# Kernel tuning notes

Measured on AMD Instinct MI355X. Metric: run time of the kernel, lower is better.

The kernel has to match this reference:

```python
import jax, jax.numpy as jnp
import numpy as np

N_NODES = 100000
N_EDGES = 625000
D_IN = 128
D_OUT = 128


def setup_inputs() -> dict:
    key = jax.random.key(0)
    k1, k2, k3, k4, k5 = jax.random.split(key, 5)
    scale = 1.0 / np.sqrt(D_IN)
    x = jax.random.normal(k1, (N_NODES, D_IN), dtype=jnp.float32)
    edge_index = jax.random.randint(k2, (2, N_EDGES), 0, N_NODES, dtype=jnp.int64)
    W_l = jax.random.normal(k3, (D_IN, D_OUT), dtype=jnp.float32) * scale
    b_l = jax.random.normal(k4, (D_OUT,), dtype=jnp.float32) * scale
    W_r = jax.random.normal(k5, (D_IN, D_OUT), dtype=jnp.float32) * scale
    return {"x": x, "edge_index": edge_index, "W_l": W_l, "b_l": b_l, "W_r": W_r}


def reference(x, edge_index, W_l, b_l, W_r):
    # SAGEConv (mean aggr, no self loops):
    #   out = lin_l(mean_{j in N(i)} x_j) + lin_r(x_i)
    src = edge_index[0]  # message source nodes
    dst = edge_index[1]  # aggregation targets
    n = x.shape[0]
    msgs = x[src]  # [E, D_IN] gather
    agg = jax.ops.segment_sum(msgs, dst, num_segments=n)  # [N, D_IN]
    deg = jax.ops.segment_sum(jnp.ones_like(dst, dtype=x.dtype), dst, num_segments=n)
    mean = agg / jnp.maximum(deg, 1.0)[:, None]  # isolated nodes -> 0
    return mean @ W_l + b_l + x @ W_r
```

## Files before the change

### kernel.cpp

```cpp
#include <hip/hip_runtime.h>


constexpr int N_NODES = 100000;
constexpr int N_EDGES = 625000;
constexpr int D = 128;
constexpr int SCAN_CHUNK = 1024;
constexpr int N_SCAN_BLOCKS = (N_NODES + SCAN_CHUNK - 1) / SCAN_CHUNK;
constexpr int CONV_BLOCKS = N_NODES * D / (512 * 4);

typedef __attribute__((ext_vector_type(8))) short short8;
typedef __attribute__((ext_vector_type(4))) short short4v;
typedef __attribute__((ext_vector_type(4))) float f32x4;

__device__ __forceinline__ unsigned short f2bf(float f) {
    union { float f; unsigned int u; } c; c.f = f;
    unsigned int u = c.u + 0x7fffu + ((c.u >> 16) & 1u);
    return (unsigned short)(u >> 16);
}
__device__ __forceinline__ float bflo(unsigned int v) {
    union { unsigned int u; float f; } c; c.u = v << 16; return c.f;
}
__device__ __forceinline__ float bfhi(unsigned int v) {
    union { unsigned int u; float f; } c; c.u = v & 0xffff0000u; return c.f;
}
__device__ __forceinline__ uint2 pack4(float4 a) {
    uint2 r;
    r.x = (unsigned)f2bf(a.x) | ((unsigned)f2bf(a.y) << 16);
    r.y = (unsigned)f2bf(a.z) | ((unsigned)f2bf(a.w) << 16);
    return r;
}

__global__ __launch_bounds__(256) void zero_cnt(int* __restrict__ cnt)
{
    int i = blockIdx.x * 256 + threadIdx.x;
    if (i < N_NODES / 4) ((uint4*)cnt)[i] = make_uint4(0, 0, 0, 0);
}

__global__ __launch_bounds__(256) void prep_hist(
    const float* __restrict__ x, const float* __restrict__ Wl,
    const float* __restrict__ Wr, const int* __restrict__ dst,
    unsigned short* __restrict__ xb, unsigned short* __restrict__ wT,
    int* __restrict__ cnt)
{
    const int tid = threadIdx.x;
    if (blockIdx.x < CONV_BLOCKS) {
        const float4* xp = (const float4*)x;
        int i1 = blockIdx.x * 512 + tid;
        int i2 = i1 + 256;
        float4 a = xp[i1];
        float4 b = xp[i2];
        ((uint2*)xb)[i1] = pack4(a);
        ((uint2*)xb)[i2] = pack4(b);
    } else {
        int t2 = (blockIdx.x - CONV_BLOCKS) * 256 + tid;
        if (t2 < 4096) {
            int n  = t2 >> 5;
            int k0 = (t2 & 31) * 8;
            short8 v;
            #pragma unroll
            for (int j = 0; j < 8; ++j) {
                int k = k0 + j;
                float f = (k < 128) ? Wl[k * 128 + n] : Wr[(k - 128) * 128 + n];
                v[j] = (short)f2bf(f);
            }
            *(short8*)&wT[n * 256 + k0] = v;
        } else if (t2 < 4096 + N_EDGES) {
            int e = t2 - 4096;
            atomicAdd(&cnt[dst[e]], 1);
        }
    }
}

__global__ __launch_bounds__(256) void csr_hist(
    const int* __restrict__ dst, int* __restrict__ cnt)
{
    int e = blockIdx.x * 256 + threadIdx.x;
    if (e < N_EDGES) atomicAdd(&cnt[dst[e]], 1);
}

__global__ __launch_bounds__(256) void scan_blocks(
    const int* __restrict__ cnt, int* __restrict__ ptr, int* __restrict__ bsums)
{
    __shared__ int sh[256];
    const int t = threadIdx.x;
    const int base = blockIdx.x * SCAN_CHUNK + t * 4;
    int v0 = (base + 0 < N_NODES) ? cnt[base + 0] : 0;
    int v1 = (base + 1 < N_NODES) ? cnt[base + 1] : 0;
    int v2 = (base + 2 < N_NODES) ? cnt[base + 2] : 0;
    int v3 = (base + 3 < N_NODES) ? cnt[base + 3] : 0;
    const int tsum = v0 + v1 + v2 + v3;
    sh[t] = tsum;
    __syncthreads();
    #pragma unroll
    for (int off = 1; off < 256; off <<= 1) {
        int val = (t >= off) ? sh[t - off] : 0;
        __syncthreads();
        sh[t] += val;
        __syncthreads();
    }
    const int texcl = sh[t] - tsum;
    if (t == 255) bsums[blockIdx.x] = sh[255];
    int e0 = texcl, e1 = e0 + v0, e2 = e1 + v1, e3 = e2 + v2;
    if (base + 0 < N_NODES) ptr[base + 0] = e0;
    if (base + 1 < N_NODES) ptr[base + 1] = e1;
    if (base + 2 < N_NODES) ptr[base + 2] = e2;
    if (base + 3 < N_NODES) ptr[base + 3] = e3;
}

__global__ __launch_bounds__(256) void add_offsets_fused(
    int* __restrict__ ptr, int* __restrict__ cursor, const int* __restrict__ bsums)
{
    __shared__ int sh[256];
    const int t = threadIdx.x;
    int v = (t < blockIdx.x) ? bsums[t] : 0;
    sh[t] = v;
    __syncthreads();
    #pragma unroll
    for (int off = 128; off > 0; off >>= 1) {
        if (t < off) sh[t] += sh[t + off];
        __syncthreads();
    }
    const int soff = sh[0];
    const int base = blockIdx.x * SCAN_CHUNK + t * 4;
    #pragma unroll
    for (int j = 0; j < 4; ++j) {
        int i = base + j;
        if (i < N_NODES) {
            int p = ptr[i] + soff;
            ptr[i] = p;
            cursor[i] = p;
        }
    }
    if (blockIdx.x == 0 && t == 0) ptr[N_NODES] = N_EDGES;
}

__global__ __launch_bounds__(256) void csr_fill(
    const int* __restrict__ src, const int* __restrict__ dst,
    int* __restrict__ cursor, int* __restrict__ sorted_src)
{
    int e = blockIdx.x * 256 + threadIdx.x;
    if (e < N_EDGES) {
        int t = dst[e];
        int pos = atomicAdd(&cursor[t], 1);
        sorted_src[pos] = src[e];
    }
}

template<bool MBF>
__global__ __launch_bounds__(256) void sage_aggregate_bf(
    const unsigned short* __restrict__ xb,
    const int* __restrict__ ptr,
    const int* __restrict__ sorted_src,
    unsigned short* __restrict__ mean_bf,
    float* __restrict__ mean_f32)
{
    const int node = blockIdx.x * 16 + (threadIdx.x >> 4);
    if (node >= N_NODES) return;
    const int l = threadIdx.x & 15;
    const int beg = ptr[node];
    const int end = ptr[node + 1];
    const size_t off = (size_t)l * 8;

    float a0=0,a1=0,a2=0,a3=0,a4=0,a5=0,a6=0,a7=0;
    float b0=0,b1=0,b2=0,b3=0,b4=0,b5=0,b6=0,b7=0;
    float c0=0,c1=0,c2=0,c3=0,c4=0,c5=0,c6=0,c7=0;
    float d0=0,d1=0,d2=0,d3=0,d4=0,d5=0,d6=0,d7=0;

    for (int i = beg; i < end; i += 4) {
        int last = end - 1;
        int e1 = i + 1 < end ? i + 1 : last;
        int e2 = i + 2 < end ? i + 2 : last;
        int e3 = i + 3 < end ? i + 3 : last;
        float w1 = (i + 1 < end) ? 1.f : 0.f;
        float w2 = (i + 2 < end) ? 1.f : 0.f;
        float w3 = (i + 3 < end) ? 1.f : 0.f;
        int s0 = sorted_src[i],  s1 = sorted_src[e1];
        int s2 = sorted_src[e2], s3 = sorted_src[e3];
        uint4 v0 = *(const uint4*)&xb[(size_t)s0 * D + off];
        uint4 v1 = *(const uint4*)&xb[(size_t)s1 * D + off];
        uint4 v2 = *(const uint4*)&xb[(size_t)s2 * D + off];
        uint4 v3 = *(const uint4*)&xb[(size_t)s3 * D + off];
        a0+=bflo(v0.x); a1+=bfhi(v0.x); a2+=bflo(v0.y); a3+=bfhi(v0.y);
        a4+=bflo(v0.z); a5+=bfhi(v0.z); a6+=bflo(v0.w); a7+=bfhi(v0.w);
        b0=fmaf(w1,bflo(v1.x),b0); b1=fmaf(w1,bfhi(v1.x),b1);
        b2=fmaf(w1,bflo(v1.y),b2); b3=fmaf(w1,bfhi(v1.y),b3);
        b4=fmaf(w1,bflo(v1.z),b4); b5=fmaf(w1,bfhi(v1.z),b5);
        b6=fmaf(w1,bflo(v1.w),b6); b7=fmaf(w1,bfhi(v1.w),b7);
        c0=fmaf(w2,bflo(v2.x),c0); c1=fmaf(w2,bfhi(v2.x),c1);
        c2=fmaf(w2,bflo(v2.y),c2); c3=fmaf(w2,bfhi(v2.y),c3);
        c4=fmaf(w2,bflo(v2.z),c4); c5=fmaf(w2,bfhi(v2.z),c5);
        c6=fmaf(w2,bflo(v2.w),c6); c7=fmaf(w2,bfhi(v2.w),c7);
        d0=fmaf(w3,bflo(v3.x),d0); d1=fmaf(w3,bfhi(v3.x),d1);
        d2=fmaf(w3,bflo(v3.y),d2); d3=fmaf(w3,bfhi(v3.y),d3);
        d4=fmaf(w3,bflo(v3.z),d4); d5=fmaf(w3,bfhi(v3.z),d5);
        d6=fmaf(w3,bflo(v3.w),d6); d7=fmaf(w3,bfhi(v3.w),d7);
    }
    const float sc = 1.0f / fmaxf((float)(end - beg), 1.0f);
    float r0 = ((a0+b0)+(c0+d0))*sc, r1 = ((a1+b1)+(c1+d1))*sc;
    float r2 = ((a2+b2)+(c2+d2))*sc, r3 = ((a3+b3)+(c3+d3))*sc;
    float r4 = ((a4+b4)+(c4+d4))*sc, r5 = ((a5+b5)+(c5+d5))*sc;
    float r6 = ((a6+b6)+(c6+d6))*sc, r7 = ((a7+b7)+(c7+d7))*sc;

    if constexpr (MBF) {
        uint4 o;
        o.x = (unsigned)f2bf(r0) | ((unsigned)f2bf(r1) << 16);
        o.y = (unsigned)f2bf(r2) | ((unsigned)f2bf(r3) << 16);
        o.z = (unsigned)f2bf(r4) | ((unsigned)f2bf(r5) << 16);
        o.w = (unsigned)f2bf(r6) | ((unsigned)f2bf(r7) << 16);
        *(uint4*)&mean_bf[(size_t)node * D + off] = o;
    } else {
        *(float4*)&mean_f32[(size_t)node * D + off] = make_float4(r0, r1, r2, r3);
        *(float4*)&mean_f32[(size_t)node * D + off + 4] = make_float4(r4, r5, r6, r7);
    }
}

__global__ __launch_bounds__(256) void sage_gemm_rb(
    const unsigned short* __restrict__ xb,
    const unsigned short* __restrict__ mean_bf,
    const unsigned short* __restrict__ wT,
    const float* __restrict__ bl,
    float* __restrict__ out)
{
    __shared__ unsigned short sA[32 * 256];

    const int tid  = threadIdx.x;
    const int lane = tid & 63;
    const int w    = tid >> 6;
    const int l15  = lane & 15;
    const int lg   = lane >> 4;

    const int n0 = w * 32 + l15;
    const int n1 = n0 + 16;

    short8 B0[8], B1[8];
    #pragma unroll
    for (int s = 0; s < 8; ++s) {
        B0[s] = *(const short8*)&wT[(size_t)n0 * 256 + s * 32 + lg * 8];
        B1[s] = *(const short8*)&wT[(size_t)n1 * 256 + s * 32 + lg * 8];
    }

    const int a_r0 = l15;
    const int a_r1 = 16 + l15;
    const float bias0 = bl[n0];
    const float bias1 = bl[n1];

    const int nTiles = N_NODES / 32;

    for (int tile = blockIdx.x; tile < nTiles; tile += gridDim.x) {
        const int row0 = tile * 32;

        #pragma unroll
        for (int i = 0; i < 4; ++i) {
            int c = tid + i * 256;
            int r = c >> 5;
            int s = c & 31;
            const unsigned short* srcp = (s < 16)
                ? &mean_bf[(size_t)(row0 + r) * D + s * 8]
                : &xb[(size_t)(row0 + r) * D + (s - 16) * 8];
            short8 v = *(const short8*)srcp;
            *(short8*)&sA[r * 256 + ((s ^ (r & 7)) << 3)] = v;
        }
        __syncthreads();

        f32x4 acc00 = {0.f,0.f,0.f,0.f}, acc01 = {0.f,0.f,0.f,0.f};
        f32x4 acc10 = {0.f,0.f,0.f,0.f}, acc11 = {0.f,0.f,0.f,0.f};

        #pragma unroll
        for (int s = 0; s < 8; ++s) {
            int ks = s * 4 + lg;
            short8 a0 = *(const short8*)&sA[a_r0 * 256 + ((ks ^ (a_r0 & 7)) << 3)];
            short8 a1 = *(const short8*)&sA[a_r1 * 256 + ((ks ^ (a_r1 & 7)) << 3)];
            acc00 = __builtin_amdgcn_mfma_f32_16x16x32_bf16(a0, B0[s], acc00, 0, 0, 0);
            acc01 = __builtin_amdgcn_mfma_f32_16x16x32_bf16(a0, B1[s], acc01, 0, 0, 0);
            acc10 = __builtin_amdgcn_mfma_f32_16x16x32_bf16(a1, B0[s], acc10, 0, 0, 0);
            acc11 = __builtin_amdgcn_mfma_f32_16x16x32_bf16(a1, B1[s], acc11, 0, 0, 0);
        }
        __syncthreads();

        #pragma unroll
        for (int reg = 0; reg < 4; ++reg) {
            int r0w = row0 + lg * 4 + reg;
            int r1w = r0w + 16;
            out[(size_t)r0w * D + n0] = acc00[reg] + bias0;
            out[(size_t)r0w * D + n1] = acc01[reg] + bias1;
            out[(size_t)r1w * D + n0] = acc10[reg] + bias0;
            out[(size_t)r1w * D + n1] = acc11[reg] + bias1;
        }
    }
}

__global__ __launch_bounds__(256) void wt_build(
    const float* __restrict__ Wl, const float* __restrict__ Wr,
    unsigned short* __restrict__ wT)
{
    int idx = blockIdx.x * 256 + threadIdx.x;
    if (idx >= 128 * 256) return;
    int n = idx >> 8;
    int k = idx & 255;
    float v = (k < 128) ? Wl[k * 128 + n] : Wr[(k - 128) * 128 + n];
    wT[n * 256 + k] = f2bf(v);
}

__global__ __launch_bounds__(256) void sage_aggregate(
    const float* __restrict__ x,
    const int* __restrict__ ptr,
    const int* __restrict__ sorted_src,
    float* __restrict__ mean)
{
    const int node = blockIdx.x * 4 + (threadIdx.x >> 6);
    if (node >= N_NODES) return;
    const int lane = threadIdx.x & 63;
    const int beg = ptr[node];
    const int end = ptr[node + 1];

    float2 acc0 = make_float2(0.f, 0.f);
    float2 acc1 = make_float2(0.f, 0.f);
    int i = beg;
    for (; i + 1 < end; i += 2) {
        int s0 = sorted_src[i];
        int s1 = sorted_src[i + 1];
        float2 a = *(const float2*)&x[(size_t)s0 * D + lane * 2];
        float2 b = *(const float2*)&x[(size_t)s1 * D + lane * 2];
        acc0.x += a.x; acc0.y += a.y;
        acc1.x += b.x; acc1.y += b.y;
    }
    if (i < end) {
        int s0 = sorted_src[i];
        float2 a = *(const float2*)&x[(size_t)s0 * D + lane * 2];
        acc0.x += a.x; acc0.y += a.y;
    }
    const float sc = 1.0f / fmaxf((float)(end - beg), 1.0f);
    float2 r = make_float2((acc0.x + acc1.x) * sc, (acc0.y + acc1.y) * sc);
    *(float2*)&mean[(size_t)node * D + lane * 2] = r;
}

__global__ __launch_bounds__(256) void sage_gemm_mfma(
    const float* __restrict__ x,
    const unsigned short* __restrict__ wT,
    const float* __restrict__ bl,
    float* __restrict__ out)
{
    __shared__ unsigned short sW[128 * 256];
    __shared__ unsigned short sA[32 * 256];

    const int tid  = threadIdx.x;
    const int lane = tid & 63;
    const int w    = tid >> 6;
    const int l15  = lane & 15;
    const int lg   = lane >> 4;

    #pragma unroll
    for (int i = 0; i < 16; ++i) {
        int c  = tid + i * 256;
        int n  = c >> 5;
        int k8 = c & 31;
        short8 v = ((const short8*)wT)[c];
        *(short8*)&sW[n * 256 + ((k8 ^ (n & 7)) << 3)] = v;
    }

    const int a_r0 = l15;
    const int a_r1 = 16 + l15;
    const int n0 = w * 32 + l15;
    const int n1 = n0 + 16;
    const float bias0 = bl[n0];
    const float bias1 = bl[n1];
    const int nTiles = N_NODES / 32;

    for (int tile = blockIdx.x; tile < nTiles; tile += gridDim.x) {
        const int row0 = tile * 32;
        #pragma unroll
        for (int i = 0; i < 8; ++i) {
            int c    = tid + i * 256;
            int r    = c >> 6;
            int half = (c >> 5) & 1;
            int f4   = c & 31;
            const float* srcp = half ? &x[(size_t)(row0 + r) * D + f4 * 4]
                                     : &out[(size_t)(row0 + r) * D + f4 * 4];
            float4 v = *(const float4*)srcp;
            short4v b;
            b.x = (short)f2bf(v.x); b.y = (short)f2bf(v.y);
            b.z = (short)f2bf(v.z); b.w = (short)f2bf(v.w);
            int k = half * 128 + f4 * 4;
            int u = k >> 3;
            *(short4v*)&sA[r * 256 + ((u ^ (r & 7)) << 3) + (k & 7)] = b;
        }
        __syncthreads();

        f32x4 acc00 = {0.f,0.f,0.f,0.f}, acc01 = {0.f,0.f,0.f,0.f};
        f32x4 acc10 = {0.f,0.f,0.f,0.f}, acc11 = {0.f,0.f,0.f,0.f};

        #pragma unroll
        for (int s = 0; s < 8; ++s) {
            int ks = s * 4 + lg;
            short8 a0 = *(const short8*)&sA[a_r0 * 256 + ((ks ^ (a_r0 & 7)) << 3)];
            short8 a1 = *(const short8*)&sA[a_r1 * 256 + ((ks ^ (a_r1 & 7)) << 3)];
            short8 b0 = *(const short8*)&sW[n0 * 256 + ((ks ^ (n0 & 7)) << 3)];
            short8 b1 = *(const short8*)&sW[n1 * 256 + ((ks ^ (n1 & 7)) << 3)];
            acc00 = __builtin_amdgcn_mfma_f32_16x16x32_bf16(a0, b0, acc00, 0, 0, 0);
            acc01 = __builtin_amdgcn_mfma_f32_16x16x32_bf16(a0, b1, acc01, 0, 0, 0);
            acc10 = __builtin_amdgcn_mfma_f32_16x16x32_bf16(a1, b0, acc10, 0, 0, 0);
            acc11 = __builtin_amdgcn_mfma_f32_16x16x32_bf16(a1, b1, acc11, 0, 0, 0);
        }
        __syncthreads();

        #pragma unroll
        for (int reg = 0; reg < 4; ++reg) {
            int r0w = row0 + lg * 4 + reg;
            int r1w = r0w + 16;
            out[(size_t)r0w * D + n0] = acc00[reg] + bias0;
            out[(size_t)r0w * D + n1] = acc01[reg] + bias1;
            out[(size_t)r1w * D + n0] = acc10[reg] + bias0;
            out[(size_t)r1w * D + n1] = acc11[reg] + bias1;
        }
    }
}

__global__ __launch_bounds__(256) void sage_scatter(
    const float* __restrict__ x, const int* __restrict__ src,
    const int* __restrict__ dst, float* __restrict__ agg, float* __restrict__ deg)
{
    int gid = blockIdx.x * 256 + threadIdx.x;
    int e = gid >> 7;
    if (e >= N_EDGES) return;
    int d = gid & 127;
    atomicAdd(&agg[(size_t)dst[e] * D + d], x[(size_t)src[e] * D + d]);
    if (d == 0) atomicAdd(&deg[dst[e]], 1.0f);
}

__global__ __launch_bounds__(256) void apply_mean(
    float* __restrict__ agg, const float* __restrict__ deg)
{
    int gid = blockIdx.x * 256 + threadIdx.x;
    int row = gid >> 5;
    if (row >= N_NODES) return;
    float sc = 1.0f / fmaxf(deg[row], 1.0f);
    float4 v = ((float4*)agg)[gid];
    v.x *= sc; v.y *= sc; v.z *= sc; v.w *= sc;
    ((float4*)agg)[gid] = v;
}

__device__ __forceinline__ void accum_tile(
    float acc[4][4], const float (*sWf)[D], const float (*srow)[D], int h, int j4)
{
    #pragma unroll 2
    for (int k = 0; k < D; k += 4) {
        float4 w0 = *(const float4*)&sWf[k + 0][j4];
        float4 w1 = *(const float4*)&sWf[k + 1][j4];
        float4 w2 = *(const float4*)&sWf[k + 2][j4];
        float4 w3 = *(const float4*)&sWf[k + 3][j4];
        #pragma unroll
        for (int r = 0; r < 4; ++r) {
            float4 a = *(const float4*)&srow[h + r * 8][k];
            acc[r][0] = fmaf(a.x, w0.x, fmaf(a.y, w1.x, fmaf(a.z, w2.x, fmaf(a.w, w3.x, acc[r][0]))));
            acc[r][1] = fmaf(a.x, w0.y, fmaf(a.y, w1.y, fmaf(a.z, w2.y, fmaf(a.w, w3.y, acc[r][1]))));
            acc[r][2] = fmaf(a.x, w0.z, fmaf(a.y, w1.z, fmaf(a.z, w2.z, fmaf(a.w, w3.z, acc[r][2]))));
            acc[r][3] = fmaf(a.x, w0.w, fmaf(a.y, w1.w, fmaf(a.z, w2.w, fmaf(a.w, w3.w, acc[r][3]))));
        }
    }
}

__global__ __launch_bounds__(256) void sage_gemm_f32(
    const float* __restrict__ x, const float* __restrict__ Wl,
    const float* __restrict__ bl, const float* __restrict__ Wr,
    float* __restrict__ out)
{
    __shared__ float sWf[D][D];
    __shared__ float srow[32][D];
    const int tid = threadIdx.x;
    const int j4 = (tid & 31) * 4;
    const int h  = tid >> 5;
    const int nTiles = (N_NODES + 31) / 32;
    const float4 bias = *(const float4*)(bl + j4);

    for (int tile = blockIdx.x; tile < nTiles; tile += gridDim.x) {
        const int row0 = tile * 32;
        float acc[4][4];
        #pragma unroll
        for (int r = 0; r < 4; ++r)
            #pragma unroll
            for (int c = 0; c < 4; ++c) acc[r][c] = 0.0f;

        __syncthreads();
        #pragma unroll
        for (int i = 0; i < 16; ++i)
            ((float4*)sWf)[tid + i * 256] = ((const float4*)Wl)[tid + i * 256];
        #pragma unroll
        for (int i = 0; i < 4; ++i) {
            int idx = tid + i * 256, r = idx >> 5, c = idx & 31, row = row0 + r;
            float4 v = make_float4(0.f,0.f,0.f,0.f);
            if (row < N_NODES) v = ((const float4*)out)[(size_t)row * 32 + c];
            ((float4*)srow)[idx] = v;
        }
        __syncthreads();
        accum_tile(acc, sWf, srow, h, j4);

        __syncthreads();
        #pragma unroll
        for (int i = 0; i < 16; ++i)
            ((float4*)sWf)[tid + i * 256] = ((const float4*)Wr)[tid + i * 256];
        #pragma unroll
        for (int i = 0; i < 4; ++i) {
            int idx = tid + i * 256, r = idx >> 5, c = idx & 31, row = row0 + r;
            float4 v = make_float4(0.f,0.f,0.f,0.f);
            if (row < N_NODES) v = ((const float4*)x)[(size_t)row * 32 + c];
            ((float4*)srow)[idx] = v;
        }
        __syncthreads();
        accum_tile(acc, sWf, srow, h, j4);

        #pragma unroll
        for (int r = 0; r < 4; ++r) {
            int row = row0 + h + r * 8;
            if (row < N_NODES) {
                float4 v = make_float4(acc[r][0] + bias.x, acc[r][1] + bias.y,
                                       acc[r][2] + bias.z, acc[r][3] + bias.w);
                *(float4*)(out + (size_t)row * D + j4) = v;
            }
        }
    }
}

extern "C" void kernel_launch(void* const* d_in, const int* in_sizes, int n_in,
                              void* d_out, int out_size, void* d_ws, size_t ws_size,
                              hipStream_t stream) {
    const float* x   = (const float*)d_in[0];
    const int*   ei  = (const int*)d_in[1];
    const float* Wl  = (const float*)d_in[2];
    const float* bl  = (const float*)d_in[3];
    const float* Wr  = (const float*)d_in[4];
    float* out = (float*)d_out;

    const int* src = ei;
    const int* dst = ei + N_EDGES;

    int* cnt    = (int*)d_ws;
    int* ptr    = cnt + N_NODES;
    int* cursor = ptr + N_NODES + 1;
    int* bsums  = cursor + N_NODES;
    int* sorted = bsums + 128;
    size_t int_count = (size_t)(3 * N_NODES + 1 + 128 + N_EDGES);
    int_count = (int_count + 7) & ~(size_t)7;
    unsigned short* wT      = (unsigned short*)((int*)d_ws + int_count);
    unsigned short* xb      = wT + 128 * 256;
    unsigned short* mean_bf = xb + (size_t)N_NODES * D;

    size_t need_B  = int_count * sizeof(int);
    size_t need_A  = need_B + 128 * 256 * 2 + 2 * (size_t)N_NODES * D * 2;

    if (ws_size >= need_A) {
        zero_cnt<<<(N_NODES / 4 + 255) / 256, 256, 0, stream>>>(cnt);
        const int TAIL_BLOCKS = (4096 + N_EDGES + 255) / 256;
        prep_hist<<<CONV_BLOCKS + TAIL_BLOCKS, 256, 0, stream>>>(
            x, Wl, Wr, dst, xb, wT, cnt);
        scan_blocks<<<N_SCAN_BLOCKS, 256, 0, stream>>>(cnt, ptr, bsums);
        add_offsets_fused<<<N_SCAN_BLOCKS, 256, 0, stream>>>(ptr, cursor, bsums);
        csr_fill<<<(N_EDGES + 255) / 256, 256, 0, stream>>>(src, dst, cursor, sorted);
        sage_aggregate_bf<true><<<(N_NODES + 15) / 16, 256, 0, stream>>>(
            xb, ptr, sorted, mean_bf, nullptr);
        sage_gemm_rb<<<768, 256, 0, stream>>>(xb, mean_bf, wT, bl, out);
    } else if (ws_size >= need_B) {
        zero_cnt<<<(N_NODES / 4 + 255) / 256, 256, 0, stream>>>(cnt);
        csr_hist<<<(N_EDGES + 255) / 256, 256, 0, stream>>>(dst, cnt);
        scan_blocks<<<N_SCAN_BLOCKS, 256, 0, stream>>>(cnt, ptr, bsums);
        add_offsets_fused<<<N_SCAN_BLOCKS, 256, 0, stream>>>(ptr, cursor, bsums);
        csr_fill<<<(N_EDGES + 255) / 256, 256, 0, stream>>>(src, dst, cursor, sorted);
        unsigned short* wTc = (unsigned short*)cursor;
        wt_build<<<(128 * 256 + 255) / 256, 256, 0, stream>>>(Wl, Wr, wTc);
        sage_aggregate<<<(N_NODES + 3) / 4, 256, 0, stream>>>(x, ptr, sorted, out);
        sage_gemm_mfma<<<512, 256, 0, stream>>>(x, wTc, bl, out);
    } else {
        float* deg = (float*)d_ws;
        hipMemsetAsync(out, 0, (size_t)N_NODES * D * sizeof(float), stream);
        hipMemsetAsync(deg, 0, (size_t)N_NODES * sizeof(float), stream);
        long long total = (long long)N_EDGES * 128;
        sage_scatter<<<(int)((total + 255) / 256), 256, 0, stream>>>(x, src, dst, out, deg);
        apply_mean<<<(N_NODES * 32 + 255) / 256, 256, 0, stream>>>(out, deg);
        sage_gemm_f32<<<512, 256, 0, stream>>>(x, Wl, bl, Wr, out);
    }
}
```

Measured before the change: 138.3 us.

## Vectorize edge histogram/fill loads and double-buffer GEMM A tile staging

The histogram and CSR fill kernels now have each thread handle four edges through int4 loads of dst/src, which cuts thread count and load instructions while keeping per-edge atomics. The row-block GEMM double-buffers its shared A tile, staging the next tile while MFMAs run on the current one, and drops one barrier per iteration. This doubles LDS use per block (32KB), which may lower occupancy. It also relies on the edge count being divisible by 4 and on the int4 loads being aligned.

Result: no change. 138.7 us (+0.3%).

```diff
diff --git a/kernel.cpp b/kernel.cpp
--- a/kernel.cpp
+++ b/kernel.cpp
@@ -7,6 +7,7 @@
 constexpr int SCAN_CHUNK = 1024;
 constexpr int N_SCAN_BLOCKS = (N_NODES + SCAN_CHUNK - 1) / SCAN_CHUNK;
 constexpr int CONV_BLOCKS = N_NODES * D / (512 * 4);
+constexpr int E4 = N_EDGES / 4;
 
 typedef __attribute__((ext_vector_type(8))) short short8;
 typedef __attribute__((ext_vector_type(4))) short short4v;
@@ -64,9 +65,13 @@
                 v[j] = (short)f2bf(f);
             }
             *(short8*)&wT[n * 256 + k0] = v;
-        } else if (t2 < 4096 + N_EDGES) {
-            int e = t2 - 4096;
-            atomicAdd(&cnt[dst[e]], 1);
+        } else if (t2 < 4096 + E4) {
+            int e = (t2 - 4096) * 4;
+            int4 d4 = *(const int4*)&dst[e];
+            atomicAdd(&cnt[d4.x], 1);
+            atomicAdd(&cnt[d4.y], 1);
+            atomicAdd(&cnt[d4.z], 1);
+            atomicAdd(&cnt[d4.w], 1);
         }
     }
 }
@@ -74,8 +79,15 @@
 __global__ __launch_bounds__(256) void csr_hist(
     const int* __restrict__ dst, int* __restrict__ cnt)
 {
-    int e = blockIdx.x * 256 + threadIdx.x;
-    if (e < N_EDGES) atomicAdd(&cnt[dst[e]], 1);
+    int t = blockIdx.x * 256 + threadIdx.x;
+    if (t < E4) {
+        int e = t * 4;
+        int4 d4 = *(const int4*)&dst[e];
+        atomicAdd(&cnt[d4.x], 1);
+        atomicAdd(&cnt[d4.y], 1);
+        atomicAdd(&cnt[d4.z], 1);
+        atomicAdd(&cnt[d4.w], 1);
+    }
 }
 
 __global__ __launch_bounds__(256) void scan_blocks(
@@ -138,11 +150,19 @@
     const int* __restrict__ src, const int* __restrict__ dst,
     int* __restrict__ cursor, int* __restrict__ sorted_src)
 {
-    int e = blockIdx.x * 256 + threadIdx.x;
-    if (e < N_EDGES) {
-        int t = dst[e];
-        int pos = atomicAdd(&cursor[t], 1);
-        sorted_src[pos] = src[e];
+    int t = blockIdx.x * 256 + threadIdx.x;
+    if (t < E4) {
+        int e = t * 4;
+        int4 d4 = *(const int4*)&dst[e];
+        int4 s4 = *(const int4*)&src[e];
+        int p0 = atomicAdd(&cursor[d4.x], 1);
+        int p1 = atomicAdd(&cursor[d4.y], 1);
+        int p2 = atomicAdd(&cursor[d4.z], 1);
+        int p3 = atomicAdd(&cursor[d4.w], 1);
+        sorted_src[p0] = s4.x;
+        sorted_src[p1] = s4.y;
+        sorted_src[p2] = s4.z;
+        sorted_src[p3] = s4.w;
     }
 }
 
@@ -221,7 +241,7 @@
     const float* __restrict__ bl,
     float* __restrict__ out)
 {
-    __shared__ unsigned short sA[32 * 256];
+    __shared__ unsigned short sA[2][32 * 256];
 
     const int tid  = threadIdx.x;
     const int lane = tid & 63;
@@ -246,9 +266,8 @@
 
     const int nTiles = N_NODES / 32;
 
-    for (int tile = blockIdx.x; tile < nTiles; tile += gridDim.x) {
+    auto stage = [&](int buf, int tile) {
         const int row0 = tile * 32;
-
         #pragma unroll
         for (int i = 0; i < 4; ++i) {
             int c = tid + i * 256;
@@ -258,9 +277,18 @@
                 ? &mean_bf[(size_t)(row0 + r) * D + s * 8]
                 : &xb[(size_t)(row0 + r) * D + (s - 16) * 8];
             short8 v = *(const short8*)srcp;
-            *(short8*)&sA[r * 256 + ((s ^ (r & 7)) << 3)] = v;
-        }
-        __syncthreads();
+            *(short8*)&sA[buf][r * 256 + ((s ^ (r & 7)) << 3)] = v;
+        }
+    };
+
+    int tile = blockIdx.x;
+    if (tile < nTiles) stage(0, tile);
+    int buf = 0;
+
+    for (; tile < nTiles; tile += gridDim.x) {
+        __syncthreads();
+        int nxt = tile + gridDim.x;
+        if (nxt < nTiles) stage(buf ^ 1, nxt);
 
         f32x4 acc00 = {0.f,0.f,0.f,0.f}, acc01 = {0.f,0.f,0.f,0.f};
         f32x4 acc10 = {0.f,0.f,0.f,0.f}, acc11 = {0.f,0.f,0.f,0.f};
@@ -268,15 +296,15 @@
         #pragma unroll
         for (int s = 0; s < 8; ++s) {
             int ks = s * 4 + lg;
-            short8 a0 = *(const short8*)&sA[a_r0 * 256 + ((ks ^ (a_r0 & 7)) << 3)];
-            short8 a1 = *(const short8*)&sA[a_r1 * 256 + ((ks ^ (a_r1 & 7)) << 3)];
+            short8 a0 = *(const short8*)&sA[buf][a_r0 * 256 + ((ks ^ (a_r0 & 7)) << 3)];
+            short8 a1 = *(const short8*)&sA[buf][a_r1 * 256 + ((ks ^ (a_r1 & 7)) << 3)];
             acc00 = __builtin_amdgcn_mfma_f32_16x16x32_bf16(a0, B0[s], acc00, 0, 0, 0);
             acc01 = __builtin_amdgcn_mfma_f32_16x16x32_bf16(a0, B1[s], acc01, 0, 0, 0);
             acc10 = __builtin_amdgcn_mfma_f32_16x16x32_bf16(a1, B0[s], acc10, 0, 0, 0);
             acc11 = __builtin_amdgcn_mfma_f32_16x16x32_bf16(a1, B1[s], acc11, 0, 0, 0);
         }
-        __syncthreads();
-
+
+        const int row0 = tile * 32;
         #pragma unroll
         for (int reg = 0; reg < 4; ++reg) {
             int r0w = row0 + lg * 4 + reg;
@@ -286,6 +314,7 @@
             out[(size_t)r1w * D + n0] = acc10[reg] + bias0;
             out[(size_t)r1w * D + n1] = acc11[reg] + bias1;
         }
+        buf ^= 1;
     }
 }
 
@@ -341,7 +370,7 @@
     float* __restrict__ out)
 {
     __shared__ unsigned short sW[128 * 256];
-    __shared__ unsigned short sA[32 * 256];
+    __shared__ unsigned short sA1[32 * 256];
 
     const int tid  = threadIdx.x;
     const int lane = tid & 63;
@@ -382,7 +411,7 @@
             b.z = (short)f2bf(v.z); b.w = (short)f2bf(v.w);
             int k = half * 128 + f4 * 4;
             int u = k >> 3;
-            *(short4v*)&sA[r * 256 + ((u ^ (r & 7)) << 3) + (k & 7)] = b;
+            *(short4v*)&sA1[r * 256 + ((u ^ (r & 7)) << 3) + (k & 7)] = b;
         }
         __syncthreads();
 
@@ -392,8 +421,8 @@
         #pragma unroll
         for (int s = 0; s < 8; ++s) {
             int ks = s * 4 + lg;
-            short8 a0 = *(const short8*)&sA[a_r0 * 256 + ((ks ^ (a_r0 & 7)) << 3)];
-            short8 a1 = *(const short8*)&sA[a_r1 * 256 + ((ks ^ (a_r1 & 7)) << 3)];
+            short8 a0 = *(const short8*)&sA1[a_r0 * 256 + ((ks ^ (a_r0 & 7)) << 3)];
+            short8 a1 = *(const short8*)&sA1[a_r1 * 256 + ((ks ^ (a_r1 & 7)) << 3)];
             short8 b0 = *(const short8*)&sW[n0 * 256 + ((ks ^ (n0 & 7)) << 3)];
             short8 b1 = *(const short8*)&sW[n1 * 256 + ((ks ^ (n1 & 7)) << 3)];
             acc00 = __builtin_amdgcn_mfma_f32_16x16x32_bf16(a0, b0, acc00, 0, 0, 0);
@@ -549,21 +578,21 @@
 
     if (ws_size >= need_A) {
         zero_cnt<<<(N_NODES / 4 + 255) / 256, 256, 0, stream>>>(cnt);
-        const int TAIL_BLOCKS = (4096 + N_EDGES + 255) / 256;
+        const int TAIL_BLOCKS = (4096 + E4 + 255) / 256;
         prep_hist<<<CONV_BLOCKS + TAIL_BLOCKS, 256, 0, stream>>>(
             x, Wl, Wr, dst, xb, wT, cnt);
         scan_blocks<<<N_SCAN_BLOCKS, 256, 0, stream>>>(cnt, ptr, bsums);
         add_offsets_fused<<<N_SCAN_BLOCKS, 256, 0, stream>>>(ptr, cursor, bsums);
-        csr_fill<<<(N_EDGES + 255) / 256, 256, 0, stream>>>(src, dst, cursor, sorted);
+        csr_fill<<<(E4 + 255) / 256, 256, 0, stream>>>(src, dst, cursor, sorted);
         sage_aggregate_bf<true><<<(N_NODES + 15) / 16, 256, 0, stream>>>(
             xb, ptr, sorted, mean_bf, nullptr);
         sage_gemm_rb<<<768, 256, 0, stream>>>(xb, mean_bf, wT, bl, out);
     } else if (ws_size >= need_B) {
         zero_cnt<<<(N_NODES / 4 + 255) / 256, 256, 0, stream>>>(cnt);
-        csr_hist<<<(N_EDGES + 255) / 256, 256, 0, stream>>>(dst, cnt);
+        csr_hist<<<(E4 + 255) / 256, 256, 0, stream>>>(dst, cnt);
         scan_blocks<<<N_SCAN_BLOCKS, 256, 0, stream>>>(cnt, ptr, bsums);
         add_offsets_fused<<<N_SCAN_BLOCKS, 256, 0, stream>>>(ptr, cursor, bsums);
-        csr_fill<<<(N_EDGES + 255) / 256, 256, 0, stream>>>(src, dst, cursor, sorted);
+        csr_fill<<<(E4 + 255) / 256, 256, 0, stream>>>(src, dst, cursor, sorted);
         unsigned short* wTc = (unsigned short*)cursor;
         wt_build<<<(128 * 256 + 255) / 256, 256, 0, stream>>>(Wl, Wr, wTc);
         sage_aggregate<<<(N_NODES + 3) / 4, 256, 0, stream>>>(x, ptr, sorted, out);
```
